# Optimization experiments

Hardware: AMD Instinct MI355X
Metric: run time of the kernel (lower is better)

Reference implementation:

```python
import jax, jax.numpy as jnp
import numpy as np

N_NODES, N_EDGES = 10000, 160000
MUL0, MUL1 = 64, 32  # multiplicities of 0e and 1o in irreps_in
AVG_DEGREE = 16.0

# ---- real-basis Wigner 3j symbols (unit Frobenius norm, as in e3nn) ----
def _su2_gen(l):
    m = np.arange(-l, l + 1)
    Jz = np.diag(m).astype(complex)
    c = np.sqrt(l * (l + 1) - m[:-1] * (m[:-1] + 1))
    Jp = np.zeros((2 * l + 1, 2 * l + 1), complex)
    Jp[np.arange(1, 2 * l + 1), np.arange(2 * l)] = c
    Jm = Jp.conj().T
    return (Jp + Jm) / 2, (Jp - Jm) / 2j, Jz

def _c2r(l):
    U = np.zeros((2 * l + 1, 2 * l + 1), complex)
    s2 = 1 / np.sqrt(2)
    for m in range(-l, l + 1):
        if m > 0:
            U[l + m, l - m] = s2; U[l + m, l + m] = (-1) ** m * s2
        elif m == 0:
            U[l, l] = 1.0
        else:
            U[l + m, l + m] = 1j * s2; U[l + m, l - m] = -1j * (-1) ** m * s2
    return U

def _real_gen(l):
    U = _c2r(l)
    return [np.real(U @ (-1j * J) @ U.conj().T) for J in _su2_gen(l)]

def real_w3j(l1, l2, l3):
    A1, A2, A3 = _real_gen(l1), _real_gen(l2), _real_gen(l3)
    d1, d2, d3 = 2 * l1 + 1, 2 * l2 + 1, 2 * l3 + 1
    I1, I2, I3 = np.eye(d1), np.eye(d2), np.eye(d3)
    M = np.concatenate([
        np.kron(np.kron(A1[k], I2), I3) + np.kron(np.kron(I1, A2[k]), I3)
        + np.kron(np.kron(I1, I2), A3[k]) for k in range(3)], 0)
    v = np.linalg.svd(M)[2][-1]
    v = v / np.linalg.norm(v)
    nz = np.nonzero(np.abs(v) > 1e-8)[0][0]
    if v[nz] < 0:
        v = -v
    return jnp.asarray(v.reshape(d1, d2, d3), dtype=jnp.float32)

W000 = real_w3j(0, 0, 0); W011 = real_w3j(0, 1, 1); W022 = real_w3j(0, 2, 2)
W101 = real_w3j(1, 0, 1); W110 = real_w3j(1, 1, 0); W112 = real_w3j(1, 1, 2)
W121 = real_w3j(1, 2, 1)

# silu second-moment normalization constant (e3nn normalize2mom)
_x, _w = np.polynomial.hermite_e.hermegauss(128)
_s = _x / (1 + np.exp(-_x))
SILU_C = float(1.0 / np.sqrt((_w * _s ** 2).sum() / _w.sum()))
SQ3, SQ5 = float(np.sqrt(3.0)), float(np.sqrt(5.0))


def _forward(node_input, node_attr, edge_attr, edge_length_embedded,
             sc_w0, sc_w1, lin1_w0, lin1_w1, fc_w0, fc_w1,
             lin2_w0, lin2_w1, lin2_w2, edge_src, edge_dst):
    N = node_input.shape[0]
    E = edge_attr.shape[0]
    a = node_attr  # [N,1] scalar (0e) node attribute
    x0 = node_input[:, :MUL0]                       # [N,64]  0e block
    x1 = node_input[:, MUL0:].reshape(N, MUL1, 3)   # [N,32,3] 1o block

    # self connection sc = FullyConnectedTensorProduct(in, attr, out); no 2e path
    s0 = (x0 @ sc_w0) * a / jnp.sqrt(float(MUL0))
    s1 = jnp.einsum('nui,uv->nvi', x1, sc_w1) * a[:, :, None] / jnp.sqrt(float(MUL1))
    s = jnp.concatenate([s0, s1.reshape(N, -1),
                         jnp.zeros((N, 32 * 5), node_input.dtype)], 1)  # [N,320]

    # lin1 = FullyConnectedTensorProduct(in, attr, in)
    y0 = (x0 @ lin1_w0) * a / jnp.sqrt(float(MUL0))
    y1 = jnp.einsum('nui,uv->nvi', x1, lin1_w1) * a[:, :, None] / jnp.sqrt(float(MUL1))

    # radial FC net -> per-edge tensor-product weights [E,320]
    h = jax.nn.silu(edge_length_embedded @ fc_w0 / jnp.sqrt(8.0)) * SILU_C
    w = h @ fc_w1 / jnp.sqrt(64.0)

    xs0 = y0[edge_src][:, :, None]  # [E,64,1]
    xs1 = y1[edge_src]              # [E,32,3]
    e0, e1, e2 = edge_attr[:, :1], edge_attr[:, 1:4], edge_attr[:, 4:9]

    def path(x, e, wgt, C, pw):
        # x:[E,u,d1] e:[E,d2] wgt:[E,u] C:[d1,d2,d3] -> [E,u,d3]
        return pw * jnp.einsum('eui,ej,ijk,eu->euk', x, e, C, wgt)

    # 7 'uvu' instructions; weight slices in instruction order, outputs in sorted
    # irreps_mid order: 64x0e,32x0e,64x1o,32x1o,32x1o,64x2e,32x2e
    k0 = path(xs0, e0, w[:, 0:64],    W000, 1.0)   # 0e x 0e -> 0e, mul 64
    k2 = path(xs0, e1, w[:, 64:128],  W011, SQ3)   # 0e x 1o -> 1o, mul 64
    k5 = path(xs0, e2, w[:, 128:192], W022, SQ5)   # 0e x 2e -> 2e, mul 64
    k3 = path(xs1, e0, w[:, 192:224], W101, SQ3)   # 1o x 0e -> 1o, mul 32
    k1 = path(xs1, e1, w[:, 224:256], W110, 1.0)   # 1o x 1o -> 0e, mul 32
    k6 = path(xs1, e1, w[:, 256:288], W112, SQ5)   # 1o x 1o -> 2e, mul 32
    k4 = path(xs1, e2, w[:, 288:320], W121, SQ3)   # 1o x 2e -> 1o, mul 32
    edge_feat = jnp.concatenate(
        [k0.reshape(E, -1), k1.reshape(E, -1), k2.reshape(E, -1), k3.reshape(E, -1),
         k4.reshape(E, -1), k5.reshape(E, -1), k6.reshape(E, -1)], 1)  # [E,960]

    agg = jax.ops.segment_sum(edge_feat, edge_dst, num_segments=N) / jnp.sqrt(AVG_DEGREE)

    # lin2 = FullyConnectedTensorProduct(mid, attr, out); per-l fused matmuls
    m0 = agg[:, :96]                        # 0e muls 64+32
    m1 = agg[:, 96:480].reshape(N, 128, 3)  # 1o muls 64+32+32
    m2 = agg[:, 480:960].reshape(N, 96, 5)  # 2e muls 64+32
    o0 = (m0 @ lin2_w0) * a / jnp.sqrt(96.0)
    o1 = jnp.einsum('nui,uv->nvi', m1, lin2_w1) * a[:, :, None] / jnp.sqrt(128.0)
    o2 = jnp.einsum('nui,uv->nvi', m2, lin2_w2) * a[:, :, None] / jnp.sqrt(96.0)
    xo = jnp.concatenate([o0, o1.reshape(N, -1), o2.reshape(N, -1)], 1)  # [N,320]

    c_s = jnp.sin(jnp.pi / 8)
    c_x = jnp.cos(jnp.pi / 8)
    mask = jnp.concatenate([jnp.ones(160), jnp.zeros(160)]).astype(node_input.dtype)
    return c_s * s + (1.0 - mask + c_x * mask) * xo


def setup_inputs() -> dict:
    key = jax.random.key(0)
    ks = jax.random.split(key, 16)
    f = jax.random.normal
    return {
        'node_input': f(ks[0], (N_NODES, 160), jnp.float32),
        'node_attr': jnp.ones((N_NODES, 1), jnp.float32),
        'edge_src': jax.random.randint(ks[1], (N_EDGES,), 0, N_NODES, dtype=jnp.int32),
        'edge_dst': jax.random.randint(ks[2], (N_EDGES,), 0, N_NODES, dtype=jnp.int32),
        'edge_attr': f(ks[3], (N_EDGES, 9), jnp.float32),
        'edge_length_embedded': jax.random.uniform(ks[4], (N_EDGES, 8), dtype=jnp.float32),
        'sc_w0': f(ks[5], (64, 64), jnp.float32),
        'sc_w1': f(ks[6], (32, 32), jnp.float32),
        'lin1_w0': f(ks[7], (64, 64), jnp.float32),
        'lin1_w1': f(ks[8], (32, 32), jnp.float32),
        'fc_w0': f(ks[9], (8, 64), jnp.float32),
        'fc_w1': f(ks[10], (64, 320), jnp.float32),
        'lin2_w0': f(ks[11], (96, 64), jnp.float32),
        'lin2_w1': f(ks[12], (128, 32), jnp.float32),
        'lin2_w2': f(ks[13], (96, 32), jnp.float32),
    }


def reference(node_input, node_attr, edge_src, edge_dst, edge_attr, edge_length_embedded,
              sc_w0, sc_w1, lin1_w0, lin1_w1, fc_w0, fc_w1, lin2_w0, lin2_w1, lin2_w2):
    return _forward(node_input, node_attr, edge_attr, edge_length_embedded,
                    sc_w0, sc_w1, lin1_w0, lin1_w1, fc_w0, fc_w1,
                    lin2_w0, lin2_w1, lin2_w2, edge_src, edge_dst)
```

## Files before the change

kernel.cpp:

```cpp
#include <hip/hip_runtime.h>
#include <cstddef>
#include <cstdint>

#define N_NODES 10000
#define N_EDGES 160000

#define RS8    0.35355339059327373f
#define RS32   0.17677669529663687f
#define RS96   0.10206207261596575f
#define RS128  0.08838834764831845f
#define RS3    0.5773502691896258f
#define SQ3_   1.7320508075688772f
#define SQ5_   2.23606797749979f
#define A_     0.18257418583505536f
#define B_     0.31622776601683794f
#define SILU_C_ 1.6765208f
#define CS_    0.3826834323650898f
#define CX_    0.9238795325112867f
#define QDEG   0.25f

typedef __attribute__((ext_vector_type(8))) short bf16x8;
typedef __attribute__((ext_vector_type(4))) float f32x4;

__device__ inline float bf2f(unsigned v) {
  union { unsigned u; float f; } c; c.u = v << 16; return c.f;
}
__device__ inline float bfhi(unsigned v) {
  union { unsigned u; float f; } c; c.u = v & 0xffff0000u; return c.f;
}
__device__ inline unsigned short f2bf(float f) {
  union { float f; unsigned u; } c; c.f = f;
  unsigned r = c.u + 0x7fff + ((c.u >> 16) & 1);
  return (unsigned short)(r >> 16);
}
__device__ inline unsigned pack2bf(float a, float b) {
  return (unsigned)f2bf(a) | ((unsigned)f2bf(b) << 16);
}

__global__ void k_init(int* __restrict__ counts, const float* __restrict__ fc1,
                       unsigned short* __restrict__ fc1p) {
  int i = blockIdx.x * blockDim.x + threadIdx.x;
  if (i < N_NODES) counts[i] = 0;
  if (i < 20480) {
    int j = i & 7, q = (i >> 3) & 3, n = (i >> 5) & 15, kq = (i >> 9) & 1, t = i >> 10;
    int k = kq * 32 + q * 8 + j;
    fc1p[i] = f2bf(fc1[k * 320 + t * 16 + n]);
  }
}

__global__ void k_hist(const int* __restrict__ edst, int* __restrict__ counts) {
  int e = blockIdx.x * blockDim.x + threadIdx.x;
  if (e < N_EDGES) atomicAdd(&counts[edst[e]], 1);
}

__global__ __launch_bounds__(256) void k_wprep(
    const float* __restrict__ sc_w0, const float* __restrict__ sc_w1,
    const float* __restrict__ w0, const float* __restrict__ w1,
    const float* __restrict__ w2, unsigned short* __restrict__ Wp) {
  int i = blockIdx.x * 256 + threadIdx.x;
  if (i >= 358400) return;
  int j = i & 7;
  int lane = (i >> 3) & 63;
  int ch = lane & 15, quad = lane >> 4;
  int r = i >> 9;
  int nt = r / 35, ks = r - nt * 35;
  int k = ks * 32 + quad * 8 + j;
  int oc = nt * 16 + ch;
  float v = 0.f;
  if (k < 96) {
    if (oc < 64) v = (CX_ * RS96) * w0[k * 64 + oc];
  } else if (k < 480) {
    int tt = k - 96, u = tt / 3, ii = tt - u * 3;
    if (oc >= 64 && oc < 160) {
      int d = oc - 64, vv = d / 3, jj = d - vv * 3;
      if (jj == ii) v = (CX_ * RS128) * w1[u * 32 + vv];
    }
  } else if (k < 960) {
    int tt = k - 480, u = tt / 5, kk = tt - u * 5;
    if (oc >= 160) {
      int d = oc - 160, vv = d / 5, jj = d - vv * 5;
      if (jj == kk) v = RS96 * w2[u * 32 + vv];
    }
  } else if (k < 1024) {
    int u = k - 960;
    if (oc < 64) v = (CS_ * 0.125f) * sc_w0[u * 64 + oc];
  } else {
    int tt = k - 1024, u = tt / 3, ii = tt - u * 3;
    if (oc >= 64 && oc < 160) {
      int d = oc - 64, vv = d / 3, jj = d - vv * 3;
      if (jj == ii) v = (CS_ * RS32) * sc_w1[u * 32 + vv];
    }
  }
  Wp[i] = f2bf(v);
}

__global__ __launch_bounds__(256) void k_scan(const int* __restrict__ counts,
                                              int* __restrict__ offs,
                                              int* __restrict__ cur,
                                              int* __restrict__ dcur) {
  __shared__ int ps[256];
  __shared__ int dbin[256];
  int t = threadIdx.x;
  dbin[t] = 0;
  int base = t * 40;
  int sum = 0;
  for (int i = 0; i < 40; ++i) {
    int idx = base + i;
    if (idx < N_NODES) sum += counts[idx];
  }
  ps[t] = sum;
  __syncthreads();
  for (int off = 1; off < 256; off <<= 1) {
    int v = (t >= off) ? ps[t - off] : 0;
    __syncthreads();
    ps[t] += v;
    __syncthreads();
  }
  int run = (t == 0) ? 0 : ps[t - 1];
  for (int i = 0; i < 40; ++i) {
    int idx = base + i;
    if (idx < N_NODES) {
      int c = counts[idx];
      offs[idx] = run; cur[idx] = run;
      run += c;
      atomicAdd(&dbin[c < 255 ? c : 255], 1);
    }
  }
  __syncthreads();
  int rb = 255 - t;
  int v = dbin[rb];
  __syncthreads();
  ps[t] = v;
  __syncthreads();
  for (int off = 1; off < 256; off <<= 1) {
    int u = (t >= off) ? ps[t - off] : 0;
    __syncthreads();
    ps[t] += u;
    __syncthreads();
  }
  dcur[rb] = ps[t] - v;
}

__global__ __launch_bounds__(256) void k_perm(
    const int* __restrict__ edst, int* __restrict__ cur,
    const int* __restrict__ counts, const int* __restrict__ offs,
    int* __restrict__ dcur, int* __restrict__ order,
    int* __restrict__ obeg, int* __restrict__ ocnt,
    const float* __restrict__ ele, const float* __restrict__ eattr,
    const int* __restrict__ esrc, float* __restrict__ ed2) {
  __shared__ __align__(16) float sh_ea[256 * 9];
  __shared__ __align__(16) float sh_el[256 * 8];
  int t = threadIdx.x;
  int eb = blockIdx.x * 256;
  int e = eb + t;
  for (int i = t; i < 2304; i += 256) sh_ea[i] = eattr[(size_t)eb * 9 + i];
  {
    const float4* src = (const float4*)(ele + (size_t)eb * 8);
    float4* dst = (float4*)sh_el;
    dst[t] = src[t]; dst[t + 256] = src[t + 256];
  }
  __syncthreads();
  int d = edst[e];
  int p = atomicAdd(&cur[d], 1);
  const float* ea = sh_ea + t * 9;
  const float* el = sh_el + t * 8;
  float4 r0 = {ea[0], ea[1], ea[2], ea[3]};
  float4 r1 = {ea[4], ea[5], ea[6], ea[7]};
  float4 r2 = {ea[8], __int_as_float(esrc[e]), 0.f, 0.f};
  float4 r3 = {el[0], el[1], el[2], el[3]};
  float4 r4 = {el[4], el[5], el[6], el[7]};
  float4* dst = (float4*)(ed2 + (size_t)p * 20);
  dst[0] = r0; dst[1] = r1; dst[2] = r2; dst[3] = r3; dst[4] = r4;
  if (e < N_NODES) {
    int c = counts[e];
    int b = c < 255 ? c : 255;
    int q = atomicAdd(&dcur[b], 1);
    order[q] = e; obeg[q] = offs[e]; ocnt[q] = c;
  }
}

__device__ inline f32x4 wtile(const unsigned short* __restrict__ fc1p,
                              bf16x8 a0, bf16x8 a1, int mrow, int quad, int t) {
  f32x4 acc = {0.f, 0.f, 0.f, 0.f};
  bf16x8 b0 = *(const bf16x8*)(fc1p + ((size_t)((t * 2 + 0) * 16 + mrow) * 4 + quad) * 8);
  bf16x8 b1 = *(const bf16x8*)(fc1p + ((size_t)((t * 2 + 1) * 16 + mrow) * 4 + quad) * 8);
  acc = __builtin_amdgcn_mfma_f32_16x16x32_bf16(b0, a0, acc, 0, 0, 0);
  acc = __builtin_amdgcn_mfma_f32_16x16x32_bf16(b1, a1, acc, 0, 0, 0);
  return acc;
}

struct WgemmShared {
  __align__(16) float ele[64][8];
  __align__(16) unsigned short h[64 * 72];
};

__device__ void w_gemm_body(WgemmShared& sh, int blk,
    const float* __restrict__ ed2, const float* __restrict__ fc0,
    const unsigned short* __restrict__ fc1p, unsigned short* __restrict__ wout) {
  int t = threadIdx.x;
  int eb = blk * 64;
  if (t < 128) {
    int e = t >> 1, hh = t & 1;
    ((float4*)&sh.ele[e][0])[hh] =
        *(const float4*)(ed2 + (size_t)(eb + e) * 20 + 12 + hh * 4);
  }
  __syncthreads();
  #pragma unroll
  for (int ii = 0; ii < 16; ++ii) {
    int idx = t + ii * 256;
    int e = idx >> 6, k = idx & 63;
    float acc = 0.f;
    #pragma unroll
    for (int m = 0; m < 8; ++m) acc += sh.ele[e][m] * fc0[m * 64 + k];
    acc *= RS8;
    float hv = SILU_C_ * acc / (1.f + __expf(-acc));
    sh.h[e * 72 + k] = f2bf(hv);
  }
  __syncthreads();

  int wv = t >> 6, lane = t & 63;
  int m0 = wv * 16;
  int mrow = lane & 15, quad = lane >> 4;
  bf16x8 a0 = *(const bf16x8*)(sh.h + (m0 + mrow) * 72 + quad * 8);
  bf16x8 a1 = *(const bf16x8*)(sh.h + (m0 + mrow) * 72 + 32 + quad * 8);
  char* wbase = (char*)wout + (size_t)(eb + m0 + mrow) * 640;
  const float K = 0.125f;
  #pragma unroll
  for (int tt = 0; tt < 4; ++tt) {
    f32x4 Av = wtile(fc1p, a0, a1, mrow, quad, tt);
    f32x4 Bv = wtile(fc1p, a0, a1, mrow, quad, tt + 4);
    uint4 st;
    st.x = pack2bf(Av[0] * K, Bv[0] * K);
    st.y = pack2bf(Av[1] * K, Bv[1] * K);
    st.z = pack2bf(Av[2] * K, Bv[2] * K);
    st.w = pack2bf(Av[3] * K, Bv[3] * K);
    *(uint4*)(wbase + 64 * tt + 16 * quad) = st;
  }
  #pragma unroll
  for (int tt = 8; tt < 12; ++tt) {
    f32x4 Cv = wtile(fc1p, a0, a1, mrow, quad, tt);
    uint2 st;
    st.x = pack2bf(Cv[0] * K, Cv[1] * K);
    st.y = pack2bf(Cv[2] * K, Cv[3] * K);
    *(uint2*)(wbase + 256 + 32 * (tt - 8) + 8 * quad) = st;
  }
  #pragma unroll
  for (int tt = 12; tt < 14; ++tt) {
    f32x4 Dv = wtile(fc1p, a0, a1, mrow, quad, tt);
    f32x4 Ev = wtile(fc1p, a0, a1, mrow, quad, tt + 2);
    f32x4 Fv = wtile(fc1p, a0, a1, mrow, quad, tt + 4);
    f32x4 Gv = wtile(fc1p, a0, a1, mrow, quad, tt + 6);
    char* db = wbase + 384 + 128 * (tt - 12) + 32 * quad;
    uint4 s0, s1;
    s0.x = pack2bf(Dv[0] * K, Ev[0] * K); s0.y = pack2bf(Fv[0] * K, Gv[0] * K);
    s0.z = pack2bf(Dv[1] * K, Ev[1] * K); s0.w = pack2bf(Fv[1] * K, Gv[1] * K);
    s1.x = pack2bf(Dv[2] * K, Ev[2] * K); s1.y = pack2bf(Fv[2] * K, Gv[2] * K);
    s1.z = pack2bf(Dv[3] * K, Ev[3] * K); s1.w = pack2bf(Fv[3] * K, Gv[3] * K);
    *(uint4*)(db) = s0;
    *(uint4*)(db + 16) = s1;
  }
}

__device__ void node_pre_body(int blk,
    const float* __restrict__ xin, const float* __restrict__ attr,
    const float* __restrict__ l1_w0, const float* __restrict__ l1_w1,
    float* __restrict__ y) {
  int idx = blk * 256 + threadIdx.x;
  int n = idx / 160, c = idx - n * 160;
  const float* xr = xin + (size_t)n * 160;
  float a = attr[n];
  if (c < 64) {
    float y_ = 0.f;
    #pragma unroll 8
    for (int u = 0; u < 64; ++u) y_ += xr[u] * l1_w0[u * 64 + c];
    y[(size_t)n * 192 + c] = y_ * a * 0.125f;
  } else {
    int t = c - 64; int v = t / 3, i = t - v * 3;
    float y_ = 0.f;
    #pragma unroll 8
    for (int u = 0; u < 32; ++u) y_ += xr[64 + u * 3 + i] * l1_w1[u * 32 + v];
    y[(size_t)n * 192 + 64 + v * 4 + i] = y_ * a * RS32;
    if (i == 2) y[(size_t)n * 192 + 64 + v * 4 + 3] = 0.f;
  }
}

__global__ __launch_bounds__(256) void k_mid(
    const float* __restrict__ ed2, const float* __restrict__ fc0,
    const unsigned short* __restrict__ fc1p, unsigned short* __restrict__ wout,
    const float* __restrict__ xin, const float* __restrict__ attr,
    const float* __restrict__ l1_w0, const float* __restrict__ l1_w1,
    float* __restrict__ y) {
  __shared__ WgemmShared sh;
  if (blockIdx.x < 2500) {
    w_gemm_body(sh, blockIdx.x, ed2, fc0, fc1p, wout);
  } else {
    node_pre_body(blockIdx.x - 2500, xin, attr, l1_w0, l1_w1, y);
  }
}

__global__ __launch_bounds__(256) void node_agg(
    const float* __restrict__ y, const float* __restrict__ ed2,
    const unsigned short* __restrict__ wbuf,
    const int* __restrict__ order, const int* __restrict__ obeg,
    const int* __restrict__ ocnt, unsigned short* __restrict__ aggb) {
  int tid = threadIdx.x, wid = tid >> 6, lane = tid & 63, l31 = lane & 31;
  int gw = blockIdx.x * 4 + wid;
  int voY  = 4 * lane;
  int voX  = 256 + 16 * l31;
  int voAB = 4 * lane;
  int voC  = 256 + 2 * lane;
  int voDG = 384 + 8 * l31;

#define E_LOAD(S, idx)                                                         \
  if ((idx) < cnt) {                                                           \
    const float4* ep = (const float4*)(ed2 + (size_t)(beg + (idx)) * 20);      \
    PE0##S = ep[0]; PE1##S = ep[1]; PE2##S = ep[2];                            \
  }
#define V_LOAD(S, idx)                                                         \
  if ((idx) < cnt) {                                                           \
    int srcn = __float_as_int(PE2##S.y);                                       \
    const char* yb = (const char*)y + (size_t)srcn * 768;                      \
    Y##S = *(const float*)(yb + voY);                                          \
    X##S = *(const f32x4*)(yb + voX);                                          \
    const char* wb = (const char*)wbuf + (size_t)(beg + (idx)) * 640;          \
    AB##S = *(const unsigned*)(wb + voAB);                                     \
    Cw##S = *(const unsigned short*)(wb + voC);                                \
    DG##S = *(const uint2*)(wb + voDG);                                        \
  }
#define COMPUTE(S)                                                             \
  {                                                                            \
    float e0 = PE0##S.x, ey = PE0##S.y, ez = PE0##S.z, ex = PE0##S.w;          \
    float q0 = PE1##S.x, q1 = PE1##S.y, q2 = PE1##S.z, q3 = PE1##S.w;          \
    float q4 = PE2##S.x;                                                       \
    float Yv = Y##S, x0 = X##S.x, x1 = X##S.y, x2 = X##S.z;                    \
    float vA = bf2f(AB##S), vB = bfhi(AB##S), vC = bf2f(Cw##S);                \
    float vD = bf2f(DG##S.x), vE = bfhi(DG##S.x);                              \
    float vF = bf2f(DG##S.y), vG = bfhi(DG##S.y);                              \
    aK0 += Yv * e0 * vA;                                                       \
    float tB = Yv * vB; aK2x += tB * ey; aK2y += tB * ez; aK2z += tB * ex;     \
    float tC = Yv * vC;                                                        \
    aK5a += tC * q0; aK5b += tC * q1; aK5c += tC * q2;                         \
    aK5d += tC * q3; aK5e += tC * q4;                                          \
    float t1 = x0 * ey + x1 * ez + x2 * ex; aK1 += (RS3 * vE) * t1;            \
    float s3 = e0 * vD; aK3x += x0 * s3; aK3y += x1 * s3; aK3z += x2 * s3;     \
    float s4 = SQ3_ * vG;                                                      \
    aK4x += s4 * (B_ * (x2 * q0 + x1 * q1 - x0 * q4) - A_ * x0 * q2);          \
    aK4y += s4 * (B_ * (x0 * q1 + x2 * q3) + 2.f * A_ * x1 * q2);              \
    aK4z += s4 * (B_ * (x0 * q0 + x1 * q3 + x2 * q4) - A_ * x2 * q2);          \
    float s6 = SQ5_ * vF;                                                      \
    aK6a += s6 * (-B_ * (x0 * ex + x2 * ey));                                  \
    aK6b += s6 * (-B_ * (x0 * ez + x1 * ey));                                  \
    aK6c += s6 * ( A_ * (x0 * ey + x2 * ex - 2.f * x1 * ez));                  \
    aK6d += s6 * (-B_ * (x1 * ex + x2 * ez));                                  \
    aK6e += s6 * ( B_ * (x0 * ey - x2 * ex));                                  \
  }

  int n = order[gw], beg = obeg[gw], cnt = ocnt[gw];

  float aK0 = 0.f, aK2x = 0.f, aK2y = 0.f, aK2z = 0.f;
  float aK5a = 0.f, aK5b = 0.f, aK5c = 0.f, aK5d = 0.f, aK5e = 0.f;
  float aK1 = 0.f, aK3x = 0.f, aK3y = 0.f, aK3z = 0.f;
  float aK4x = 0.f, aK4y = 0.f, aK4z = 0.f;
  float aK6a = 0.f, aK6b = 0.f, aK6c = 0.f, aK6d = 0.f, aK6e = 0.f;

  float4 PE0a, PE1a, PE2a, PE0b, PE1b, PE2b;
  float Ya, Yb; f32x4 Xa, Xb;
  unsigned ABa, ABb; unsigned short Cwa, Cwb;
  uint2 DGa, DGb;

  E_LOAD(a, 0)
  E_LOAD(b, 1)
  V_LOAD(a, 0)

  int i = 0;
  while (i < cnt) {
    V_LOAD(b, i + 1)
    COMPUTE(a)
    E_LOAD(a, i + 2)
    ++i; if (i >= cnt) break;
    V_LOAD(a, i + 1)
    COMPUTE(b)
    E_LOAD(b, i + 2)
    ++i;
  }

  unsigned short* ag = aggb + (size_t)n * 960;
  ag[lane]           = f2bf(aK0  * QDEG);
  ag[96 + 3 * lane]  = f2bf(aK2x * QDEG);
  ag[97 + 3 * lane]  = f2bf(aK2y * QDEG);
  ag[98 + 3 * lane]  = f2bf(aK2z * QDEG);
  ag[480 + 5 * lane] = f2bf(aK5a * QDEG);
  ag[481 + 5 * lane] = f2bf(aK5b * QDEG);
  ag[482 + 5 * lane] = f2bf(aK5c * QDEG);
  ag[483 + 5 * lane] = f2bf(aK5d * QDEG);
  ag[484 + 5 * lane] = f2bf(aK5e * QDEG);
  if (lane < 32) {
    ag[64 + lane]      = f2bf(aK1  * QDEG);
    ag[288 + 3 * lane] = f2bf(aK3x * QDEG);
    ag[289 + 3 * lane] = f2bf(aK3y * QDEG);
    ag[290 + 3 * lane] = f2bf(aK3z * QDEG);
    ag[384 + 3 * lane] = f2bf(aK4x * QDEG);
    ag[385 + 3 * lane] = f2bf(aK4y * QDEG);
    ag[386 + 3 * lane] = f2bf(aK4z * QDEG);
    ag[800 + 5 * lane] = f2bf(aK6a * QDEG);
    ag[801 + 5 * lane] = f2bf(aK6b * QDEG);
    ag[802 + 5 * lane] = f2bf(aK6c * QDEG);
    ag[803 + 5 * lane] = f2bf(aK6d * QDEG);
    ag[804 + 5 * lane] = f2bf(aK6e * QDEG);
  }
#undef E_LOAD
#undef V_LOAD
#undef COMPUTE
}

#define ASTR 1128
__global__ __launch_bounds__(256) void k_out(
    const unsigned short* __restrict__ aggb, const float* __restrict__ xin,
    const float* __restrict__ attr, const unsigned short* __restrict__ Wp,
    float* __restrict__ out) {
  __shared__ __align__(16) unsigned short Ash[16 * ASTR];
  int t = threadIdx.x;
  int nbase = blockIdx.x * 16;
  for (int idx = t; idx < 16 * 480; idx += 256) {
    int row = idx / 480, c = idx - row * 480;
    *(unsigned*)(Ash + row * ASTR + 2 * c) =
        *(const unsigned*)(aggb + (size_t)(nbase + row) * 960 + 2 * c);
  }
  for (int idx = t; idx < 16 * 80; idx += 256) {
    int row = idx / 80, c = idx - row * 80;
    const float* xp = xin + (size_t)(nbase + row) * 160 + 2 * c;
    *(unsigned*)(Ash + row * ASTR + 960 + 2 * c) = pack2bf(xp[0], xp[1]);
  }
  __syncthreads();

  int wid = t >> 6, lane = t & 63;
  int ch = lane & 15, quad = lane >> 4;
  f32x4 acc0 = {0.f,0.f,0.f,0.f}, acc1 = {0.f,0.f,0.f,0.f};
  f32x4 acc2 = {0.f,0.f,0.f,0.f}, acc3 = {0.f,0.f,0.f,0.f};
  f32x4 acc4 = {0.f,0.f,0.f,0.f};
  const unsigned short* arow = Ash + ch * ASTR + quad * 8;
  const unsigned short* wq0 = Wp + ((size_t)(wid * 5 + 0) * 35 * 64 + lane) * 8;
  const unsigned short* wq1 = Wp + ((size_t)(wid * 5 + 1) * 35 * 64 + lane) * 8;
  const unsigned short* wq2 = Wp + ((size_t)(wid * 5 + 2) * 35 * 64 + lane) * 8;
  const unsigned short* wq3 = Wp + ((size_t)(wid * 5 + 3) * 35 * 64 + lane) * 8;
  const unsigned short* wq4 = Wp + ((size_t)(wid * 5 + 4) * 35 * 64 + lane) * 8;
  for (int ks = 0; ks < 35; ++ks) {
    bf16x8 af = *(const bf16x8*)(arow + ks * 32);
    bf16x8 w0f = *(const bf16x8*)(wq0 + ks * 512);
    bf16x8 w1f = *(const bf16x8*)(wq1 + ks * 512);
    bf16x8 w2f = *(const bf16x8*)(wq2 + ks * 512);
    bf16x8 w3f = *(const bf16x8*)(wq3 + ks * 512);
    bf16x8 w4f = *(const bf16x8*)(wq4 + ks * 512);
    acc0 = __builtin_amdgcn_mfma_f32_16x16x32_bf16(w0f, af, acc0, 0, 0, 0);
    acc1 = __builtin_amdgcn_mfma_f32_16x16x32_bf16(w1f, af, acc1, 0, 0, 0);
    acc2 = __builtin_amdgcn_mfma_f32_16x16x32_bf16(w2f, af, acc2, 0, 0, 0);
    acc3 = __builtin_amdgcn_mfma_f32_16x16x32_bf16(w3f, af, acc3, 0, 0, 0);
    acc4 = __builtin_amdgcn_mfma_f32_16x16x32_bf16(w4f, af, acc4, 0, 0, 0);
  }
  float a = attr[nbase + ch];
  float* orow = out + (size_t)(nbase + ch) * 320 + quad * 4;
  {
    float4 st = {acc0[0]*a, acc0[1]*a, acc0[2]*a, acc0[3]*a};
    *(float4*)(orow + (wid * 5 + 0) * 16) = st;
  }
  {
    float4 st = {acc1[0]*a, acc1[1]*a, acc1[2]*a, acc1[3]*a};
    *(float4*)(orow + (wid * 5 + 1) * 16) = st;
  }
  {
    float4 st = {acc2[0]*a, acc2[1]*a, acc2[2]*a, acc2[3]*a};
    *(float4*)(orow + (wid * 5 + 2) * 16) = st;
  }
  {
    float4 st = {acc3[0]*a, acc3[1]*a, acc3[2]*a, acc3[3]*a};
    *(float4*)(orow + (wid * 5 + 3) * 16) = st;
  }
  {
    float4 st = {acc4[0]*a, acc4[1]*a, acc4[2]*a, acc4[3]*a};
    *(float4*)(orow + (wid * 5 + 4) * 16) = st;
  }
}

extern "C" void kernel_launch(void* const* d_in, const int* in_sizes, int n_in,
                              void* d_out, int out_size, void* d_ws, size_t ws_size,
                              hipStream_t stream) {
  const float* node_input = (const float*)d_in[0];
  const float* node_attr  = (const float*)d_in[1];
  const int*   edge_src   = (const int*)d_in[2];
  const int*   edge_dst   = (const int*)d_in[3];
  const float* edge_attr  = (const float*)d_in[4];
  const float* ele        = (const float*)d_in[5];
  const float* sc_w0      = (const float*)d_in[6];
  const float* sc_w1      = (const float*)d_in[7];
  const float* l1_w0      = (const float*)d_in[8];
  const float* l1_w1      = (const float*)d_in[9];
  const float* fc_w0      = (const float*)d_in[10];
  const float* fc_w1      = (const float*)d_in[11];
  const float* l2_w0      = (const float*)d_in[12];
  const float* l2_w1      = (const float*)d_in[13];
  const float* l2_w2      = (const float*)d_in[14];
  float* out = (float*)d_out;

  char* base = (char*)d_ws;
  float* y              = (float*)(base);
  unsigned short* wbuf  = (unsigned short*)(base + 7680000);
  float* ed2            = (float*)(base + 110080000);
  int* counts           = (int*)(base + 122880000);
  int* offs             = (int*)(base + 122920000);
  int* cur              = (int*)(base + 122960000);
  int* order            = (int*)(base + 123000000);
  int* obeg             = (int*)(base + 123040000);
  int* ocnt             = (int*)(base + 123080000);
  int* dcur             = (int*)(base + 123120000);
  unsigned short* fc1p  = (unsigned short*)(base + 123121024);
  unsigned short* aggb  = (unsigned short*)(base + 123162624);
  unsigned short* Wp    = (unsigned short*)(base + 142362624);

  hipLaunchKernelGGL(k_init, dim3(80), dim3(256), 0, stream, counts, fc_w1, fc1p);
  hipLaunchKernelGGL(k_wprep, dim3(1400), dim3(256), 0, stream,
                     sc_w0, sc_w1, l2_w0, l2_w1, l2_w2, Wp);
  hipLaunchKernelGGL(k_hist, dim3((N_EDGES + 255) / 256), dim3(256), 0, stream,
                     edge_dst, counts);
  hipLaunchKernelGGL(k_scan, dim3(1), dim3(256), 0, stream, counts, offs, cur, dcur);
  hipLaunchKernelGGL(k_perm, dim3(N_EDGES / 256), dim3(256), 0, stream,
                     edge_dst, cur, counts, offs, dcur, order, obeg, ocnt,
                     ele, edge_attr, edge_src, ed2);
  hipLaunchKernelGGL(k_mid, dim3(2500 + 6250), dim3(256), 0, stream,
                     ed2, fc_w0, fc1p, wbuf,
                     node_input, node_attr, l1_w0, l1_w1, y);
  hipLaunchKernelGGL(node_agg, dim3(2500), dim3(256), 0, stream,
                     y, ed2, wbuf, order, obeg, ocnt, aggb);
  hipLaunchKernelGGL(k_out, dim3(625), dim3(256), 0, stream,
                     aggb, node_input, node_attr, Wp, out);
}
```

Before: 222.4 us.

## Compute node pre-linear with bf16 MFMA in separate kernel using prepacked weights

The per-node linear (lin1) was a scalar fp32 loop fused into the k_mid launch alongside the edge weight GEMM. It now runs as its own kernel k_npre, which stages node features as bf16 in LDS and uses 16x16x32 bf16 MFMA against weights prepacked by k_wprep into a block-diagonal MFMA layout. This is meant to cut the FMA and global-load cost of the scalar loop, at the price of one extra launch and bf16 rounding of the inputs and lin1 weights.

```diff
diff --git a/kernel.cpp b/kernel.cpp
--- a/kernel.cpp
+++ b/kernel.cpp
@@ -56,42 +56,65 @@
 __global__ __launch_bounds__(256) void k_wprep(
     const float* __restrict__ sc_w0, const float* __restrict__ sc_w1,
     const float* __restrict__ w0, const float* __restrict__ w1,
-    const float* __restrict__ w2, unsigned short* __restrict__ Wp) {
+    const float* __restrict__ w2, const float* __restrict__ l1_w0,
+    const float* __restrict__ l1_w1, unsigned short* __restrict__ Wp,
+    unsigned short* __restrict__ Wyp) {
   int i = blockIdx.x * 256 + threadIdx.x;
-  if (i >= 358400) return;
-  int j = i & 7;
-  int lane = (i >> 3) & 63;
-  int ch = lane & 15, quad = lane >> 4;
-  int r = i >> 9;
-  int nt = r / 35, ks = r - nt * 35;
-  int k = ks * 32 + quad * 8 + j;
-  int oc = nt * 16 + ch;
-  float v = 0.f;
-  if (k < 96) {
-    if (oc < 64) v = (CX_ * RS96) * w0[k * 64 + oc];
-  } else if (k < 480) {
-    int tt = k - 96, u = tt / 3, ii = tt - u * 3;
-    if (oc >= 64 && oc < 160) {
-      int d = oc - 64, vv = d / 3, jj = d - vv * 3;
-      if (jj == ii) v = (CX_ * RS128) * w1[u * 32 + vv];
+  if (i < 358400) {
+    int j = i & 7;
+    int lane = (i >> 3) & 63;
+    int ch = lane & 15, quad = lane >> 4;
+    int r = i >> 9;
+    int nt = r / 35, ks = r - nt * 35;
+    int k = ks * 32 + quad * 8 + j;
+    int oc = nt * 16 + ch;
+    float v = 0.f;
+    if (k < 96) {
+      if (oc < 64) v = (CX_ * RS96) * w0[k * 64 + oc];
+    } else if (k < 480) {
+      int tt = k - 96, u = tt / 3, ii = tt - u * 3;
+      if (oc >= 64 && oc < 160) {
+        int d = oc - 64, vv = d / 3, jj = d - vv * 3;
+        if (jj == ii) v = (CX_ * RS128) * w1[u * 32 + vv];
+      }
+    } else if (k < 960) {
+      int tt = k - 480, u = tt / 5, kk = tt - u * 5;
+      if (oc >= 160) {
+        int d = oc - 160, vv = d / 5, jj = d - vv * 5;
+        if (jj == kk) v = RS96 * w2[u * 32 + vv];
+      }
+    } else if (k < 1024) {
+      int u = k - 960;
+      if (oc < 64) v = (CS_ * 0.125f) * sc_w0[u * 64 + oc];
+    } else {
+      int tt = k - 1024, u = tt / 3, ii = tt - u * 3;
+      if (oc >= 64 && oc < 160) {
+        int d = oc - 64, vv = d / 3, jj = d - vv * 3;
+        if (jj == ii) v = (CS_ * RS32) * sc_w1[u * 32 + vv];
+      }
     }
-  } else if (k < 960) {
-    int tt = k - 480, u = tt / 5, kk = tt - u * 5;
-    if (oc >= 160) {
-      int d = oc - 160, vv = d / 5, jj = d - vv * 5;
-      if (jj == kk) v = RS96 * w2[u * 32 + vv];
+    Wp[i] = f2bf(v);
+  } else if (i < 358400 + 30720) {
+    int ii2 = i - 358400;
+    int j = ii2 & 7;
+    int lane = (ii2 >> 3) & 63;
+    int ch = lane & 15, quad = lane >> 4;
+    int r = ii2 >> 9;
+    int nt = r / 5, ks = r - nt * 5;
+    int k = ks * 32 + quad * 8 + j;
+    int oc = nt * 16 + ch;
+    float v = 0.f;
+    if (k < 64) {
+      if (oc < 64) v = 0.125f * l1_w0[k * 64 + oc];
+    } else {
+      int tt = k - 64, u = tt / 3, ci = tt - u * 3;
+      if (oc >= 64) {
+        int d = oc - 64, vv = d >> 2, jj = d & 3;
+        if (jj == ci) v = RS32 * l1_w1[u * 32 + vv];
+      }
     }
-  } else if (k < 1024) {
-    int u = k - 960;
-    if (oc < 64) v = (CS_ * 0.125f) * sc_w0[u * 64 + oc];
-  } else {
-    int tt = k - 1024, u = tt / 3, ii = tt - u * 3;
-    if (oc >= 64 && oc < 160) {
-      int d = oc - 64, vv = d / 3, jj = d - vv * 3;
-      if (jj == ii) v = (CS_ * RS32) * sc_w1[u * 32 + vv];
-    }
-  }
-  Wp[i] = f2bf(v);
+    Wyp[ii2] = f2bf(v);
+  }
 }
 
 __global__ __launch_bounds__(256) void k_scan(const int* __restrict__ counts,
@@ -261,41 +284,51 @@
   }
 }
 
-__device__ void node_pre_body(int blk,
-    const float* __restrict__ xin, const float* __restrict__ attr,
-    const float* __restrict__ l1_w0, const float* __restrict__ l1_w1,
-    float* __restrict__ y) {
-  int idx = blk * 256 + threadIdx.x;
-  int n = idx / 160, c = idx - n * 160;
-  const float* xr = xin + (size_t)n * 160;
-  float a = attr[n];
-  if (c < 64) {
-    float y_ = 0.f;
-    #pragma unroll 8
-    for (int u = 0; u < 64; ++u) y_ += xr[u] * l1_w0[u * 64 + c];
-    y[(size_t)n * 192 + c] = y_ * a * 0.125f;
-  } else {
-    int t = c - 64; int v = t / 3, i = t - v * 3;
-    float y_ = 0.f;
-    #pragma unroll 8
-    for (int u = 0; u < 32; ++u) y_ += xr[64 + u * 3 + i] * l1_w1[u * 32 + v];
-    y[(size_t)n * 192 + 64 + v * 4 + i] = y_ * a * RS32;
-    if (i == 2) y[(size_t)n * 192 + 64 + v * 4 + 3] = 0.f;
-  }
-}
-
 __global__ __launch_bounds__(256) void k_mid(
     const float* __restrict__ ed2, const float* __restrict__ fc0,
-    const unsigned short* __restrict__ fc1p, unsigned short* __restrict__ wout,
+    const unsigned short* __restrict__ fc1p, unsigned short* __restrict__ wout) {
+  __shared__ WgemmShared sh;
+  w_gemm_body(sh, blockIdx.x, ed2, fc0, fc1p, wout);
+}
+
+#define YSTR 168
+__global__ __launch_bounds__(256) void k_npre(
     const float* __restrict__ xin, const float* __restrict__ attr,
-    const float* __restrict__ l1_w0, const float* __restrict__ l1_w1,
-    float* __restrict__ y) {
-  __shared__ WgemmShared sh;
-  if (blockIdx.x < 2500) {
-    w_gemm_body(sh, blockIdx.x, ed2, fc0, fc1p, wout);
-  } else {
-    node_pre_body(blockIdx.x - 2500, xin, attr, l1_w0, l1_w1, y);
-  }
+    const unsigned short* __restrict__ Wyp, float* __restrict__ y) {
+  __shared__ __align__(16) unsigned short Ash[16 * YSTR];
+  int t = threadIdx.x;
+  int nbase = blockIdx.x * 16;
+  for (int idx = t; idx < 16 * 80; idx += 256) {
+    int row = idx / 80, c = idx - row * 80;
+    const float* xp = xin + (size_t)(nbase + row) * 160 + 2 * c;
+    *(unsigned*)(Ash + row * YSTR + 2 * c) = pack2bf(xp[0], xp[1]);
+  }
+  __syncthreads();
+  int wid = t >> 6, lane = t & 63;
+  int ch = lane & 15, quad = lane >> 4;
+  const unsigned short* arow = Ash + ch * YSTR + quad * 8;
+  f32x4 acc0 = {0.f,0.f,0.f,0.f}, acc1 = {0.f,0.f,0.f,0.f}, acc2 = {0.f,0.f,0.f,0.f};
+  const unsigned short* wq0 = Wyp + ((size_t)(wid * 3 + 0) * 5 * 64 + lane) * 8;
+  const unsigned short* wq1 = Wyp + ((size_t)(wid * 3 + 1) * 5 * 64 + lane) * 8;
+  const unsigned short* wq2 = Wyp + ((size_t)(wid * 3 + 2) * 5 * 64 + lane) * 8;
+  #pragma unroll
+  for (int ks = 0; ks < 5; ++ks) {
+    bf16x8 af  = *(const bf16x8*)(arow + ks * 32);
+    bf16x8 w0f = *(const bf16x8*)(wq0 + ks * 512);
+    bf16x8 w1f = *(const bf16x8*)(wq1 + ks * 512);
+    bf16x8 w2f = *(const bf16x8*)(wq2 + ks * 512);
+    acc0 = __builtin_amdgcn_mfma_f32_16x16x32_bf16(w0f, af, acc0, 0, 0, 0);
+    acc1 = __builtin_amdgcn_mfma_f32_16x16x32_bf16(w1f, af, acc1, 0, 0, 0);
+    acc2 = __builtin_amdgcn_mfma_f32_16x16x32_bf16(w2f, af, acc2, 0, 0, 0);
+  }
+  float a = attr[nbase + ch];
+  float* yrow = y + (size_t)(nbase + ch) * 192 + quad * 4;
+  { float4 st = {acc0[0]*a, acc0[1]*a, acc0[2]*a, acc0[3]*a};
+    *(float4*)(yrow + (wid * 3 + 0) * 16) = st; }
+  { float4 st = {acc1[0]*a, acc1[1]*a, acc1[2]*a, acc1[3]*a};
+    *(float4*)(yrow + (wid * 3 + 1) * 16) = st; }
+  { float4 st = {acc2[0]*a, acc2[1]*a, acc2[2]*a, acc2[3]*a};
+    *(float4*)(yrow + (wid * 3 + 2) * 16) = st; }
 }
 
 __global__ __launch_bounds__(256) void node_agg(
@@ -515,19 +548,21 @@
   unsigned short* fc1p  = (unsigned short*)(base + 123121024);
   unsigned short* aggb  = (unsigned short*)(base + 123162624);
   unsigned short* Wp    = (unsigned short*)(base + 142362624);
+  unsigned short* Wyp   = (unsigned short*)(base + 143079424);
 
   hipLaunchKernelGGL(k_init, dim3(80), dim3(256), 0, stream, counts, fc_w1, fc1p);
-  hipLaunchKernelGGL(k_wprep, dim3(1400), dim3(256), 0, stream,
-                     sc_w0, sc_w1, l2_w0, l2_w1, l2_w2, Wp);
+  hipLaunchKernelGGL(k_wprep, dim3(1520), dim3(256), 0, stream,
+                     sc_w0, sc_w1, l2_w0, l2_w1, l2_w2, l1_w0, l1_w1, Wp, Wyp);
   hipLaunchKernelGGL(k_hist, dim3((N_EDGES + 255) / 256), dim3(256), 0, stream,
                      edge_dst, counts);
   hipLaunchKernelGGL(k_scan, dim3(1), dim3(256), 0, stream, counts, offs, cur, dcur);
   hipLaunchKernelGGL(k_perm, dim3(N_EDGES / 256), dim3(256), 0, stream,
                      edge_dst, cur, counts, offs, dcur, order, obeg, ocnt,
                      ele, edge_attr, edge_src, ed2);
-  hipLaunchKernelGGL(k_mid, dim3(2500 + 6250), dim3(256), 0, stream,
-                     ed2, fc_w0, fc1p, wbuf,
-                     node_input, node_attr, l1_w0, l1_w1, y);
+  hipLaunchKernelGGL(k_npre, dim3(625), dim3(256), 0, stream,
+                     node_input, node_attr, Wyp, y);
+  hipLaunchKernelGGL(k_mid, dim3(2500), dim3(256), 0, stream,
+                     ed2, fc_w0, fc1p, wbuf);
   hipLaunchKernelGGL(node_agg, dim3(2500), dim3(256), 0, stream,
                      y, ed2, wbuf, order, obeg, ocnt, aggb);
   hipLaunchKernelGGL(k_out, dim3(625), dim3(256), 0, stream,
```

Measured after the change: 205.1 us. -7.8%, faster.
